# Performance work log

Measured on AMD Instinct MI355X. Metric: run time of the kernel, lower is better.

The kernel has to match this reference:

```python
import jax, jax.numpy as jnp
import numpy as np


def setup_inputs() -> dict:
    key = jax.random.key(0)
    ks = jax.random.split(key, 7)
    T, K, D_x, D_y = 8192, 64, 128, 64
    X = jax.random.normal(ks[0], (T, D_x), dtype=jnp.float32)
    Y = jax.random.normal(ks[1], (T, D_y), dtype=jnp.float32)
    # learned parameters (small random values for non-degenerate math)
    init_logits = jax.random.normal(ks[2], (K,), dtype=jnp.float32) * 0.1
    W = jax.random.normal(ks[3], (K, K, D_x), dtype=jnp.float32) * 0.05
    b = jax.random.normal(ks[4], (K, K), dtype=jnp.float32) * 0.1
    mu = jax.random.normal(ks[5], (K, D_y), dtype=jnp.float32) * 0.1
    log_var_unconstrained = jax.random.normal(ks[6], (K, D_y), dtype=jnp.float32) * 0.1
    return {"X": X, "Y": Y, "init_logits": init_logits, "W": W, "b": b,
            "mu": mu, "log_var_unconstrained": log_var_unconstrained}


def reference(X, Y, init_logits, W, b, mu, log_var_unconstrained):
    # log pi0
    log_pi0 = jax.nn.log_softmax(init_logits)
    # emissions for all t: diagonal Gaussian log-pdf, log_em [T, K]
    log_var = jnp.clip(log_var_unconstrained, -6.0, 6.0)  # [K, D_y]
    D = Y.shape[-1]
    LOG2PI = jnp.log(jnp.asarray(2.0 * np.pi, dtype=Y.dtype))
    diff = Y[:, None, :] - mu[None, :, :]                 # [T, K, D_y]
    quad = jnp.sum(diff * diff * jnp.exp(-log_var)[None], axis=-1)  # [T, K]
    logdet = jnp.sum(log_var, axis=-1)                    # [K]
    log_em = -0.5 * (D * LOG2PI + logdet[None, :] + quad)  # [T, K]
    # time-varying transition logits: b_ij + x_t . W_ij, row-softmax over j
    logits = b[None, :, :] + jnp.einsum('ijd,td->tij', W, X)  # [T, K, K]
    log_A = jax.nn.log_softmax(logits, axis=2)                 # [T, K, K]
    # forward recursion: alpha_t(j) = log_em_t(j) + logsumexp_i(alpha_{t-1}(i) + log_A_t(i,j))
    alpha0 = log_pi0 + log_em[0]

    def step(alpha, inputs):
        log_A_t, log_em_t = inputs
        alpha_new = log_em_t + jax.nn.logsumexp(alpha[:, None] + log_A_t, axis=0)
        return alpha_new, None

    alpha_T, _ = jax.lax.scan(step, alpha0, (log_A[1:], log_em[1:]))
    loglik = jax.nn.logsumexp(alpha_T)
    return loglik
```

## Files before the change

### kernel.cpp

```cpp
#include <hip/hip_runtime.h>
#include <hip/hip_bf16.h>


typedef unsigned int u32;
typedef unsigned short u16;

#define T_LEN 8192

typedef __attribute__((ext_vector_type(8))) short bf16x8;
typedef __attribute__((ext_vector_type(4))) float f32x4;

__device__ __forceinline__ float bflo(u32 u){ return __uint_as_float(u << 16); }
__device__ __forceinline__ float bfhi(u32 u){ return __uint_as_float(u & 0xffff0000u); }
__device__ __forceinline__ u32 f2bf(float x){
  u32 b = __float_as_uint(x);
  return (b + 0x7fffu + ((b >> 16) & 1u)) >> 16;
}
__device__ __forceinline__ u32 pack2bf(float a, float b){
  return f2bf(a) | (f2bf(b) << 16);
}

__device__ __forceinline__ void gld_lds16(const void* g, void* l){
#if defined(__has_builtin) && __has_builtin(__builtin_amdgcn_global_load_lds)
  __builtin_amdgcn_global_load_lds(
      (const __attribute__((address_space(1))) unsigned int*)g,
      (__attribute__((address_space(3))) unsigned int*)l, 16, 0, 0);
#else
  *(uint4*)((char*)l + (threadIdx.x & 63) * 16) = *(const uint4*)g;
#endif
}

__global__ __launch_bounds__(64) void k_prep(
    const float* __restrict__ mu, const float* __restrict__ lvu,
    float* __restrict__ muT, float* __restrict__ ivT, float* __restrict__ logdet)
{
  const int k = threadIdx.x;
  float ld = 0.f;
  for (int d = 0; d < 64; ++d){
    float lv = fminf(fmaxf(lvu[k*64 + d], -6.f), 6.f);
    ld += lv;
    muT[d*64 + k] = mu[k*64 + d];
    ivT[d*64 + k] = __expf(-lv);
  }
  logdet[k] = ld;
}

__global__ __launch_bounds__(256) void k_emis(
    const float* __restrict__ Y, const float* __restrict__ muT,
    const float* __restrict__ ivT, const float* __restrict__ logdet,
    const float* __restrict__ X, const float* __restrict__ W,
    float* __restrict__ emp, float* __restrict__ cvec,
    u16* __restrict__ Xsw, u16* __restrict__ Wsw)
{
  const int tid = threadIdx.x;
  const int w = tid >> 6, k = tid & 63;
  const int t = blockIdx.x * 4 + w;
  float y = Y[(size_t)t*64 + k];
  float quad = 0.f;
  #pragma unroll 8
  for (int d = 0; d < 64; ++d){
    float yd = __shfl(y, d, 64);
    float df = yd - muT[d*64 + k];
    quad = fmaf(df*df, ivT[d*64 + k], quad);
  }
  float le = -0.5f*(117.6241322f + logdet[k] + quad);
  float m = le;
  #pragma unroll
  for (int off = 1; off < 64; off <<= 1) m = fmaxf(m, __shfl_xor(m, off, 64));
  emp[(size_t)t*64 + k] = __expf(le - m);
  if (k == 0) cvec[t] = m;

  if (tid < 128){
    int rl = tid >> 5, c32 = tid & 31;
    int tr = blockIdx.x*4 + rl;
    float4 v = *(const float4*)(X + (size_t)tr*128 + c32*4);
    int c16 = c32 >> 1, h = c32 & 1;
    int byte = tr*256 + ((c16 ^ (tr & 7))*16 + h*8);
    *(uint2*)((char*)Xsw + byte) = make_uint2(pack2bf(v.x,v.y), pack2bf(v.z,v.w));
  }
  if (blockIdx.x < 512){
    int f4 = blockIdx.x*256 + tid;
    int r = f4 >> 5, c32 = f4 & 31;
    float4 v = *(const float4*)(W + (size_t)f4*4);
    int c16 = c32 >> 1, h = c32 & 1;
    int byte = r*256 + ((c16 ^ (r & 7))*16 + h*8);
    *(uint2*)((char*)Wsw + byte) = make_uint2(pack2bf(v.x,v.y), pack2bf(v.z,v.w));
  }
}

__global__ __launch_bounds__(256) void k_trans(
    const u16* __restrict__ Xsw, const u16* __restrict__ Wsw,
    const float* __restrict__ bmat, const float* __restrict__ emp,
    u16* __restrict__ Ap)
{
  __shared__ __align__(16) u16 Wt[128*128];
  __shared__ __align__(16) u16 Xt[64*128];
  __shared__ float Sred[8][64];
  const int tid = threadIdx.x;
  const int lane = tid & 63, w = tid >> 6;
  const int lr = lane & 15, lg = lane >> 4;
  const int t0 = blockIdx.x * 64;
  const int i0 = blockIdx.y * 2;

  {
    const char* xsrc = (const char*)(Xsw + (size_t)t0*128);
    const char* wsrc = (const char*)(Wsw + (size_t)i0*64*128);
    #pragma unroll
    for (int c = 0; c < 4; ++c){
      int kb = w*4 + c;
      gld_lds16(xsrc + kb*1024 + lane*16, (char*)Xt + kb*1024);
    }
    #pragma unroll
    for (int c = 0; c < 8; ++c){
      int kb = w*8 + c;
      gld_lds16(wsrc + kb*1024 + lane*16, (char*)Wt + kb*1024);
    }
  }
  __syncthreads();

  f32x4 acc[2][4] = {};
  #pragma unroll
  for (int kg = 0; kg < 4; ++kg){
    const int kc = kg*4 + lg;
    bf16x8 a[2], b[4];
    #pragma unroll
    for (int jt = 0; jt < 2; ++jt){
      int row = (w + jt*4)*16 + lr;
      a[jt] = *(const bf16x8*)((const char*)Wt + row*256 + ((kc ^ (row & 7))*16));
    }
    #pragma unroll
    for (int tt = 0; tt < 4; ++tt){
      int row = tt*16 + lr;
      b[tt] = *(const bf16x8*)((const char*)Xt + row*256 + ((kc ^ (row & 7))*16));
    }
    #pragma unroll
    for (int jt = 0; jt < 2; ++jt)
      #pragma unroll
      for (int tt = 0; tt < 4; ++tt)
        acc[jt][tt] = __builtin_amdgcn_mfma_f32_16x16x32_bf16(a[jt], b[tt], acc[jt][tt], 0, 0, 0);
  }

  float bvv[2][4];
  #pragma unroll
  for (int jt = 0; jt < 2; ++jt){
    int q = w + jt*4;
    int ig = i0 + (q >> 2);
    #pragma unroll
    for (int reg = 0; reg < 4; ++reg)
      bvv[jt][reg] = bmat[ig*64 + (q & 3)*16 + lg*4 + reg];
  }

  __syncthreads();
  u16* Ct = Xt;

  #pragma unroll
  for (int jt = 0; jt < 2; ++jt){
    const int q = w + jt*4;
    #pragma unroll
    for (int tt = 0; tt < 4; ++tt){
      const int t = tt*16 + lr;
      float e0 = __expf(acc[jt][tt][0] + bvv[jt][0]);
      float e1 = __expf(acc[jt][tt][1] + bvv[jt][1]);
      float e2 = __expf(acc[jt][tt][2] + bvv[jt][2]);
      float e3 = __expf(acc[jt][tt][3] + bvv[jt][3]);
      float s = e0 + e1 + e2 + e3;
      s += __shfl_xor(s, 16, 64);
      s += __shfl_xor(s, 32, 64);
      if (lg == 0) Sred[q][t] = s;
      const int byte = t*256 + ((q*32 + lg*8) ^ ((t & 7) << 4));
      *(u32*)((char*)Ct + byte)     = pack2bf(e0, e1);
      *(u32*)((char*)Ct + byte + 4) = pack2bf(e2, e3);
    }
  }
  __syncthreads();

  {
    const int trow = tid >> 2, seg = tid & 3;
    float invs[2];
    #pragma unroll
    for (int ii = 0; ii < 2; ++ii){
      float s = Sred[ii*4+0][trow] + Sred[ii*4+1][trow]
              + Sred[ii*4+2][trow] + Sred[ii*4+3][trow];
      invs[ii] = 1.0f / s;
    }
    const int sw = (trow & 7) << 4;
    u16* orow = Ap + (size_t)(t0 + trow)*4096 + i0*64;
    const float* er = emp + (size_t)(t0 + trow)*64;
    #pragma unroll
    for (int u = 0; u < 4; ++u){
      const int bcol = seg*64 + u*16;
      uint4 v = *(const uint4*)((const char*)Ct + trow*256 + (bcol ^ sw));
      const int j0 = bcol >> 1;
      const float inv = invs[j0 >> 6];
      const int je = j0 & 63;
      float4 ea = *(const float4*)(er + je);
      float4 eb = *(const float4*)(er + je + 4);
      u32 r0 = pack2bf(bflo(v.x)*inv*ea.x, bfhi(v.x)*inv*ea.y);
      u32 r1 = pack2bf(bflo(v.y)*inv*ea.z, bfhi(v.y)*inv*ea.w);
      u32 r2 = pack2bf(bflo(v.z)*inv*eb.x, bfhi(v.z)*inv*eb.y);
      u32 r3 = pack2bf(bflo(v.w)*inv*eb.z, bfhi(v.w)*inv*eb.w);
      *(uint4*)(orow + j0) = make_uint4(r0, r1, r2, r3);
    }
  }
}

__global__ __launch_bounds__(256) void k_scan(
    u16* mats, int mstride, int per_wg, int skip0,
    const float* __restrict__ in_sc, float* __restrict__ out_sc)
{
  __shared__ u32 Apk[2][32*68];
  const int tid = threadIdx.x;
  const int lane = tid & 63, w = tid >> 6;
  const int r16 = lane & 15, oct = lane >> 4;
  int c0 = blockIdx.x * per_wg, cnt = per_wg;
  const size_t out_slot = (size_t)c0 * mstride;
  if (blockIdx.x == 0){ c0 += skip0; cnt -= skip0; }

  bf16x8 Bf[2];
  {
    const u16* m0 = mats + ((size_t)c0*mstride << 12) + (w*16 + r16)*64 + oct*8;
    Bf[0] = *(const bf16x8*)(m0);
    Bf[1] = *(const bf16x8*)(m0 + 32);
  }
  float S = in_sc ? in_sc[c0*4 + w] : 0.0f;

  const int lp = tid >> 3, c8 = tid & 7;
  auto STAGE = [&](int buf, const u16* src){
    const uint4 A = *(const uint4*)(src + lp*128 + c8*8);
    const uint4 B = *(const uint4*)(src + lp*128 + 64 + c8*8);
    uint4 o0, o1;
    o0.x = (A.x & 0xffffu) | (B.x << 16);
    o0.y = (A.x >> 16)     | (B.x & 0xffff0000u);
    o0.z = (A.y & 0xffffu) | (B.y << 16);
    o0.w = (A.y >> 16)     | (B.y & 0xffff0000u);
    o1.x = (A.z & 0xffffu) | (B.z << 16);
    o1.y = (A.z >> 16)     | (B.z & 0xffff0000u);
    o1.z = (A.w & 0xffffu) | (B.w << 16);
    o1.w = (A.w >> 16)     | (B.w & 0xffff0000u);
    u32* dst = &Apk[buf][lp*68 + c8*8];
    *(uint4*)(dst)     = o0;
    *(uint4*)(dst + 4) = o1;
  };

  if (cnt > 1) STAGE(0, mats + ((size_t)(c0+1)*mstride << 12));
  __syncthreads();
  int cur = 0;
  for (int kk = 1; kk < cnt; ++kk){
    if (kk + 1 < cnt) STAGE(cur ^ 1, mats + ((size_t)(c0 + kk + 1)*mstride << 12));

    if (in_sc){
      const float* sp = in_sc + (size_t)(c0 + kk)*4;
      float s0=sp[0], s1=sp[1], s2=sp[2], s3=sp[3];
      float sm = fmaxf(fmaxf(s0,s1), fmaxf(s2,s3));
      S += sm;
      #pragma unroll
      for (int kt = 0; kt < 2; ++kt){
        float slo = (kt == 0) ? s0 : s2;
        float shi = (kt == 0) ? s1 : s3;
        float se = __expf(((oct >> 1) ? shi : slo) - sm);
        uint4 bv4 = __builtin_bit_cast(uint4, Bf[kt]);
        bv4.x = pack2bf(bflo(bv4.x)*se, bfhi(bv4.x)*se);
        bv4.y = pack2bf(bflo(bv4.y)*se, bfhi(bv4.y)*se);
        bv4.z = pack2bf(bflo(bv4.z)*se, bfhi(bv4.z)*se);
        bv4.w = pack2bf(bflo(bv4.w)*se, bfhi(bv4.w)*se);
        Bf[kt] = __builtin_bit_cast(bf16x8, bv4);
      }
    }

    f32x4 acc[4] = {};
    const u32* Ab = &Apk[cur][0];
    #pragma unroll
    for (int kt = 0; kt < 2; ++kt){
      const u32* gb = Ab + (kt*16 + oct*4)*68 + r16;
      #pragma unroll
      for (int jt = 0; jt < 4; ++jt){
        const u32* g = gb + jt*16;
        uint4 av = make_uint4(g[0], g[68], g[136], g[204]);
        acc[jt] = __builtin_amdgcn_mfma_f32_16x16x32_bf16(
            __builtin_bit_cast(bf16x8, av), Bf[kt], acc[jt], 0, 0, 0);
      }
    }

    float mx = acc[0][0];
    #pragma unroll
    for (int jt = 0; jt < 4; ++jt)
      #pragma unroll
      for (int q = 0; q < 4; ++q) mx = fmaxf(mx, acc[jt][q]);
    #pragma unroll
    for (int off = 1; off < 64; off <<= 1) mx = fmaxf(mx, __shfl_xor(mx, off, 64));
    float inv = 1.0f / mx;
    S += __logf(mx);

    u32 p0[4], p1[4];
    #pragma unroll
    for (int jt = 0; jt < 4; ++jt){
      p0[jt] = pack2bf(acc[jt][0]*inv, acc[jt][1]*inv);
      p1[jt] = pack2bf(acc[jt][2]*inv, acc[jt][3]*inv);
    }
    const int s0l = r16 + 32*(oct & 1), s1l = s0l + 16;
    const bool hi = (oct >> 1) != 0;
    #pragma unroll
    for (int kt = 0; kt < 2; ++kt){
      u32 a0 = __shfl(p0[2*kt],   s0l, 64), a1 = __shfl(p1[2*kt],   s0l, 64);
      u32 a2 = __shfl(p0[2*kt],   s1l, 64), a3 = __shfl(p1[2*kt],   s1l, 64);
      u32 b0 = __shfl(p0[2*kt+1], s0l, 64), b1 = __shfl(p1[2*kt+1], s0l, 64);
      u32 b2 = __shfl(p0[2*kt+1], s1l, 64), b3 = __shfl(p1[2*kt+1], s1l, 64);
      uint4 nb;
      nb.x = hi ? b0 : a0;
      nb.y = hi ? b1 : a1;
      nb.z = hi ? b2 : a2;
      nb.w = hi ? b3 : a3;
      Bf[kt] = __builtin_bit_cast(bf16x8, nb);
    }
    cur ^= 1;
    __syncthreads();
  }
  {
    u16* outp = mats + (out_slot << 12) + (w*16 + r16)*64 + oct*8;
    *(bf16x8*)(outp)      = Bf[0];
    *(bf16x8*)(outp + 32) = Bf[1];
    if (lane == 0) out_sc[blockIdx.x*4 + w] = S;
  }
}

__global__ __launch_bounds__(256) void k_final(
    const float* __restrict__ init_logits, const float* __restrict__ emp,
    const float* __restrict__ cvec, const u16* __restrict__ Mfin, int mstride,
    const float* __restrict__ scfin, int nmat, float* __restrict__ out)
{
  __shared__ float wsum[4];
  const int tid = threadIdx.x;
  float part = 0.f;
  for (int t = tid; t < T_LEN; t += 256) part += cvec[t];
  #pragma unroll
  for (int off = 1; off < 64; off <<= 1) part += __shfl_xor(part, off, 64);
  if ((tid & 63) == 0) wsum[tid >> 6] = part;
  __syncthreads();
  if (tid >= 64) return;
  const float csum = wsum[0] + wsum[1] + wsum[2] + wsum[3];
  const int k = tid;
  float ilv = init_logits[k];
  float m = ilv;
  #pragma unroll
  for (int off = 1; off < 64; off <<= 1) m = fmaxf(m, __shfl_xor(m, off, 64));
  float e = __expf(ilv - m);
  float s = e;
  #pragma unroll
  for (int off = 1; off < 64; off <<= 1) s += __shfl_xor(s, off, 64);
  float alpha = (e / s) * emp[k];
  float S = 0.f;
  for (int d = 0; d < nmat; ++d){
    const float* sp = scfin + d*4;
    float sm = fmaxf(fmaxf(sp[0], sp[1]), fmaxf(sp[2], sp[3]));
    alpha *= __expf(sp[k >> 4] - sm);
    S += sm;
    const u16* Mp = Mfin + ((size_t)d*mstride << 12);
    float an = 0.f;
    for (int i2 = 0; i2 < 64; ++i2){
      float av = __shfl(alpha, i2, 64);
      an = fmaf(av, __uint_as_float(((u32)Mp[i2*64 + k]) << 16), an);
    }
    float mx = an;
    #pragma unroll
    for (int off = 1; off < 64; off <<= 1) mx = fmaxf(mx, __shfl_xor(mx, off, 64));
    alpha = an / mx;
    S += __logf(mx);
  }
  float tot = alpha;
  #pragma unroll
  for (int off = 1; off < 64; off <<= 1) tot += __shfl_xor(tot, off, 64);
  if (k == 0) out[0] = __logf(tot) + S + csum;
}

extern "C" void kernel_launch(void* const* d_in, const int* in_sizes, int n_in,
                              void* d_out, int out_size, void* d_ws, size_t ws_size,
                              hipStream_t stream)
{
  const float* X  = (const float*)d_in[0];
  const float* Y  = (const float*)d_in[1];
  const float* il = (const float*)d_in[2];
  const float* W  = (const float*)d_in[3];
  const float* bm = (const float*)d_in[4];
  const float* mu = (const float*)d_in[5];
  const float* lv = (const float*)d_in[6];
  float* out = (float*)d_out;
  char* ws = (char*)d_ws;
  (void)in_sizes; (void)n_in; (void)out_size; (void)ws_size;

  float* emp    = (float*)(ws + 0x0000000);
  float* cvec   = (float*)(ws + 0x0200000);
  float* muT    = (float*)(ws + 0x0210000);
  float* ivT    = (float*)(ws + 0x0214000);
  float* logdet = (float*)(ws + 0x0218000);
  float* sc1    = (float*)(ws + 0x0220000);
  float* sc2    = (float*)(ws + 0x0224000);
  float* sc3    = (float*)(ws + 0x0225000);
  float* sc4    = (float*)(ws + 0x0226000);
  u16*   Xsw    = (u16*)  (ws + 0x0240000);
  u16*   Wsw    = (u16*)  (ws + 0x0440000);
  u16*   Ap     = (u16*)  (ws + 0x0600000);

  k_prep <<<1, 64, 0, stream>>>(mu, lv, muT, ivT, logdet);
  k_emis <<<2048, 256, 0, stream>>>(Y, muT, ivT, logdet, X, W, emp, cvec, Xsw, Wsw);
  k_trans<<<dim3(128, 32), 256, 0, stream>>>(Xsw, Wsw, bm, emp, Ap);
  k_scan <<<1024, 256, 0, stream>>>(Ap,   1,  8, 1, (const float*)nullptr, sc1);
  k_scan <<<128,  256, 0, stream>>>(Ap,   8,  8, 0, sc1, sc2);
  k_scan <<<16,   256, 0, stream>>>(Ap,  64,  8, 0, sc2, sc3);
  k_scan <<<1,    256, 0, stream>>>(Ap, 512, 16, 0, sc3, sc4);
  k_final<<<1, 256, 0, stream>>>(il, emp, cvec, Ap, 1, sc4, 1, out);
}
```

Measured before the change: 205.2 us.

## Fuse scan levels into one cooperative kernel, fold prep into emission kernel

The four scan-level launches and the final kernel are merged into one cooperative kernel that uses grid-wide syncs between tree levels, with the old multi-launch path kept as a fallback if the cooperative launch fails. The separate prep kernel is removed: each emission block now rebuilds transposed mu and inverse variances in shared memory. The transition kernel's epilogue is remapped so each wave writes contiguous 16-byte chunks of rows. The aim is to cut launch gaps and the single-block prep kernel, at the cost of redundant per-block prep work and grid-sync overhead with mostly idle blocks at the upper levels.

```diff
diff --git a/kernel.cpp b/kernel.cpp
--- a/kernel.cpp
+++ b/kernel.cpp
@@ -1,6 +1,9 @@
 #include <hip/hip_runtime.h>
 #include <hip/hip_bf16.h>
-
+#include <hip/hip_cooperative_groups.h>
+
+
+namespace cg = cooperative_groups;
 
 typedef unsigned int u32;
 typedef unsigned short u16;
@@ -30,40 +33,52 @@
 #endif
 }
 
-__global__ __launch_bounds__(64) void k_prep(
-    const float* __restrict__ mu, const float* __restrict__ lvu,
-    float* __restrict__ muT, float* __restrict__ ivT, float* __restrict__ logdet)
-{
-  const int k = threadIdx.x;
-  float ld = 0.f;
-  for (int d = 0; d < 64; ++d){
-    float lv = fminf(fmaxf(lvu[k*64 + d], -6.f), 6.f);
-    ld += lv;
-    muT[d*64 + k] = mu[k*64 + d];
-    ivT[d*64 + k] = __expf(-lv);
-  }
-  logdet[k] = ld;
-}
-
 __global__ __launch_bounds__(256) void k_emis(
-    const float* __restrict__ Y, const float* __restrict__ muT,
-    const float* __restrict__ ivT, const float* __restrict__ logdet,
+    const float* __restrict__ Y, const float* __restrict__ mu,
+    const float* __restrict__ lvu,
     const float* __restrict__ X, const float* __restrict__ W,
     float* __restrict__ emp, float* __restrict__ cvec,
     u16* __restrict__ Xsw, u16* __restrict__ Wsw)
 {
+  __shared__ float muT_s[64][65];
+  __shared__ float ivT_s[64][65];
   const int tid = threadIdx.x;
   const int w = tid >> 6, k = tid & 63;
+
+  #pragma unroll
+  for (int u = 0; u < 4; ++u){
+    int f4 = u*256 + tid;
+    int r = f4 >> 4, c4 = (f4 & 15) * 4;
+    float4 m4 = *(const float4*)(mu + (size_t)f4*4);
+    float4 l4 = *(const float4*)(lvu + (size_t)f4*4);
+    muT_s[c4+0][r] = m4.x; muT_s[c4+1][r] = m4.y;
+    muT_s[c4+2][r] = m4.z; muT_s[c4+3][r] = m4.w;
+    ivT_s[c4+0][r] = fminf(fmaxf(l4.x, -6.f), 6.f);
+    ivT_s[c4+1][r] = fminf(fmaxf(l4.y, -6.f), 6.f);
+    ivT_s[c4+2][r] = fminf(fmaxf(l4.z, -6.f), 6.f);
+    ivT_s[c4+3][r] = fminf(fmaxf(l4.w, -6.f), 6.f);
+  }
+  __syncthreads();
+  float ld = 0.f;
+  #pragma unroll 8
+  for (int d = 0; d < 64; ++d) ld += ivT_s[d][k];
+  __syncthreads();
+  if (w == 0){
+    #pragma unroll 8
+    for (int d = 0; d < 64; ++d) ivT_s[d][k] = __expf(-ivT_s[d][k]);
+  }
+  __syncthreads();
+
   const int t = blockIdx.x * 4 + w;
   float y = Y[(size_t)t*64 + k];
   float quad = 0.f;
   #pragma unroll 8
   for (int d = 0; d < 64; ++d){
     float yd = __shfl(y, d, 64);
-    float df = yd - muT[d*64 + k];
-    quad = fmaf(df*df, ivT[d*64 + k], quad);
-  }
-  float le = -0.5f*(117.6241322f + logdet[k] + quad);
+    float df = yd - muT_s[d][k];
+    quad = fmaf(df*df, ivT_s[d][k], quad);
+  }
+  float le = -0.5f*(117.6241322f + ld + quad);
   float m = le;
   #pragma unroll
   for (int off = 1; off < 64; off <<= 1) m = fmaxf(m, __shfl_xor(m, off, 64));
@@ -175,46 +190,36 @@
   __syncthreads();
 
   {
-    const int trow = tid >> 2, seg = tid & 3;
-    float invs[2];
-    #pragma unroll
-    for (int ii = 0; ii < 2; ++ii){
-      float s = Sred[ii*4+0][trow] + Sred[ii*4+1][trow]
-              + Sred[ii*4+2][trow] + Sred[ii*4+3][trow];
-      invs[ii] = 1.0f / s;
-    }
-    const int sw = (trow & 7) << 4;
-    u16* orow = Ap + (size_t)(t0 + trow)*4096 + i0*64;
-    const float* er = emp + (size_t)(t0 + trow)*64;
+    const int rl = lane >> 4;
+    const int ch = lane & 15;
+    const int h = ch >> 3;
     #pragma unroll
     for (int u = 0; u < 4; ++u){
-      const int bcol = seg*64 + u*16;
-      uint4 v = *(const uint4*)((const char*)Ct + trow*256 + (bcol ^ sw));
-      const int j0 = bcol >> 1;
-      const float inv = invs[j0 >> 6];
-      const int je = j0 & 63;
-      float4 ea = *(const float4*)(er + je);
-      float4 eb = *(const float4*)(er + je + 4);
+      const int row = w*16 + u*4 + rl;
+      float s = Sred[h*4+0][row] + Sred[h*4+1][row]
+              + Sred[h*4+2][row] + Sred[h*4+3][row];
+      const float inv = 1.0f / s;
+      uint4 v = *(const uint4*)((const char*)Ct + row*256 + ((ch*16) ^ ((row & 7) << 4)));
+      const float* er = emp + (size_t)(t0 + row)*64 + (ch & 7)*8;
+      float4 ea = *(const float4*)(er);
+      float4 eb = *(const float4*)(er + 4);
       u32 r0 = pack2bf(bflo(v.x)*inv*ea.x, bfhi(v.x)*inv*ea.y);
       u32 r1 = pack2bf(bflo(v.y)*inv*ea.z, bfhi(v.y)*inv*ea.w);
       u32 r2 = pack2bf(bflo(v.z)*inv*eb.x, bfhi(v.z)*inv*eb.y);
       u32 r3 = pack2bf(bflo(v.w)*inv*eb.z, bfhi(v.w)*inv*eb.w);
-      *(uint4*)(orow + j0) = make_uint4(r0, r1, r2, r3);
-    }
-  }
-}
-
-__global__ __launch_bounds__(256) void k_scan(
-    u16* mats, int mstride, int per_wg, int skip0,
-    const float* __restrict__ in_sc, float* __restrict__ out_sc)
-{
-  __shared__ u32 Apk[2][32*68];
-  const int tid = threadIdx.x;
+      *(uint4*)(Ap + (size_t)(t0 + row)*4096 + (size_t)i0*64 + ch*8) = make_uint4(r0, r1, r2, r3);
+    }
+  }
+}
+
+__device__ void fold_chunk(
+    u16* mats, int c0_in, int mstride, int cnt_in, int skip,
+    const float* in_sc, float* out_sc, int tid, u32 (&Apk)[2][32*68])
+{
   const int lane = tid & 63, w = tid >> 6;
   const int r16 = lane & 15, oct = lane >> 4;
-  int c0 = blockIdx.x * per_wg, cnt = per_wg;
-  const size_t out_slot = (size_t)c0 * mstride;
-  if (blockIdx.x == 0){ c0 += skip0; cnt -= skip0; }
+  int c0 = c0_in + skip, cnt = cnt_in - skip;
+  const size_t out_slot = (size_t)c0_in * mstride;
 
   bf16x8 Bf[2];
   {
@@ -319,17 +324,15 @@
     u16* outp = mats + (out_slot << 12) + (w*16 + r16)*64 + oct*8;
     *(bf16x8*)(outp)      = Bf[0];
     *(bf16x8*)(outp + 32) = Bf[1];
-    if (lane == 0) out_sc[blockIdx.x*4 + w] = S;
-  }
-}
-
-__global__ __launch_bounds__(256) void k_final(
-    const float* __restrict__ init_logits, const float* __restrict__ emp,
-    const float* __restrict__ cvec, const u16* __restrict__ Mfin, int mstride,
-    const float* __restrict__ scfin, int nmat, float* __restrict__ out)
+    if (lane == 0) out_sc[w] = S;
+  }
+}
+
+__device__ void final_ll(
+    const float* init_logits, const float* emp, const float* cvec,
+    const u16* Mfin, const float* scfin, float* out, int tid)
 {
   __shared__ float wsum[4];
-  const int tid = threadIdx.x;
   float part = 0.f;
   for (int t = tid; t < T_LEN; t += 256) part += cvec[t];
   #pragma unroll
@@ -348,28 +351,56 @@
   #pragma unroll
   for (int off = 1; off < 64; off <<= 1) s += __shfl_xor(s, off, 64);
   float alpha = (e / s) * emp[k];
-  float S = 0.f;
-  for (int d = 0; d < nmat; ++d){
-    const float* sp = scfin + d*4;
-    float sm = fmaxf(fmaxf(sp[0], sp[1]), fmaxf(sp[2], sp[3]));
-    alpha *= __expf(sp[k >> 4] - sm);
-    S += sm;
-    const u16* Mp = Mfin + ((size_t)d*mstride << 12);
-    float an = 0.f;
-    for (int i2 = 0; i2 < 64; ++i2){
-      float av = __shfl(alpha, i2, 64);
-      an = fmaf(av, __uint_as_float(((u32)Mp[i2*64 + k]) << 16), an);
-    }
-    float mx = an;
-    #pragma unroll
-    for (int off = 1; off < 64; off <<= 1) mx = fmaxf(mx, __shfl_xor(mx, off, 64));
-    alpha = an / mx;
-    S += __logf(mx);
-  }
-  float tot = alpha;
+  const float* sp = scfin;
+  float sm = fmaxf(fmaxf(sp[0], sp[1]), fmaxf(sp[2], sp[3]));
+  alpha *= __expf(sp[k >> 4] - sm);
+  float S = sm;
+  float an = 0.f;
+  for (int i2 = 0; i2 < 64; ++i2){
+    float av = __shfl(alpha, i2, 64);
+    an = fmaf(av, __uint_as_float(((u32)Mfin[i2*64 + k]) << 16), an);
+  }
+  float tot = an;
   #pragma unroll
   for (int off = 1; off < 64; off <<= 1) tot += __shfl_xor(tot, off, 64);
   if (k == 0) out[0] = __logf(tot) + S + csum;
+}
+
+__global__ __launch_bounds__(256, 4) void k_scanall(
+    u16* mats, const float* init_logits, const float* emp, const float* cvec,
+    float* sc1, float* sc2, float* sc3, float* sc4, float* out)
+{
+  __shared__ u32 Apk[2][32*68];
+  cg::grid_group grid = cg::this_grid();
+  const int b = blockIdx.x;
+  const int tid = threadIdx.x;
+  fold_chunk(mats, b*8, 1, 8, (b == 0) ? 1 : 0, nullptr, sc1 + b*4, tid, Apk);
+  grid.sync();
+  if (b < 128) fold_chunk(mats, b*8, 8, 8, 0, sc1, sc2 + b*4, tid, Apk);
+  grid.sync();
+  if (b < 16) fold_chunk(mats, b*8, 64, 8, 0, sc2, sc3 + b*4, tid, Apk);
+  grid.sync();
+  if (b == 0) fold_chunk(mats, 0, 512, 16, 0, sc3, sc4, tid, Apk);
+  grid.sync();
+  if (b == 0) final_ll(init_logits, emp, cvec, mats, sc4, out, tid);
+}
+
+__global__ __launch_bounds__(256) void k_scan_lvl(
+    u16* mats, int mstride, int per_wg, int skip0,
+    const float* __restrict__ in_sc, float* __restrict__ out_sc)
+{
+  __shared__ u32 Apk[2][32*68];
+  const int b = blockIdx.x;
+  fold_chunk(mats, b*per_wg, mstride, per_wg, (b == 0) ? skip0 : 0,
+             in_sc, out_sc + b*4, threadIdx.x, Apk);
+}
+
+__global__ __launch_bounds__(256) void k_final_k(
+    const float* __restrict__ init_logits, const float* __restrict__ emp,
+    const float* __restrict__ cvec, const u16* __restrict__ Mfin,
+    const float* __restrict__ scfin, float* __restrict__ out)
+{
+  final_ll(init_logits, emp, cvec, Mfin, scfin, out, threadIdx.x);
 }
 
 extern "C" void kernel_launch(void* const* d_in, const int* in_sizes, int n_in,
@@ -387,25 +418,28 @@
   char* ws = (char*)d_ws;
   (void)in_sizes; (void)n_in; (void)out_size; (void)ws_size;
 
-  float* emp    = (float*)(ws + 0x0000000);
-  float* cvec   = (float*)(ws + 0x0200000);
-  float* muT    = (float*)(ws + 0x0210000);
-  float* ivT    = (float*)(ws + 0x0214000);
-  float* logdet = (float*)(ws + 0x0218000);
-  float* sc1    = (float*)(ws + 0x0220000);
-  float* sc2    = (float*)(ws + 0x0224000);
-  float* sc3    = (float*)(ws + 0x0225000);
-  float* sc4    = (float*)(ws + 0x0226000);
-  u16*   Xsw    = (u16*)  (ws + 0x0240000);
-  u16*   Wsw    = (u16*)  (ws + 0x0440000);
-  u16*   Ap     = (u16*)  (ws + 0x0600000);
-
-  k_prep <<<1, 64, 0, stream>>>(mu, lv, muT, ivT, logdet);
-  k_emis <<<2048, 256, 0, stream>>>(Y, muT, ivT, logdet, X, W, emp, cvec, Xsw, Wsw);
+  float* emp  = (float*)(ws + 0x0000000);
+  float* cvec = (float*)(ws + 0x0200000);
+  float* sc1  = (float*)(ws + 0x0220000);
+  float* sc2  = (float*)(ws + 0x0224000);
+  float* sc3  = (float*)(ws + 0x0225000);
+  float* sc4  = (float*)(ws + 0x0226000);
+  u16*   Xsw  = (u16*)  (ws + 0x0240000);
+  u16*   Wsw  = (u16*)  (ws + 0x0440000);
+  u16*   Ap   = (u16*)  (ws + 0x0600000);
+
+  k_emis <<<2048, 256, 0, stream>>>(Y, mu, lv, X, W, emp, cvec, Xsw, Wsw);
   k_trans<<<dim3(128, 32), 256, 0, stream>>>(Xsw, Wsw, bm, emp, Ap);
-  k_scan <<<1024, 256, 0, stream>>>(Ap,   1,  8, 1, (const float*)nullptr, sc1);
-  k_scan <<<128,  256, 0, stream>>>(Ap,   8,  8, 0, sc1, sc2);
-  k_scan <<<16,   256, 0, stream>>>(Ap,  64,  8, 0, sc2, sc3);
-  k_scan <<<1,    256, 0, stream>>>(Ap, 512, 16, 0, sc3, sc4);
-  k_final<<<1, 256, 0, stream>>>(il, emp, cvec, Ap, 1, sc4, 1, out);
-}
+
+  void* args[] = {(void*)&Ap, (void*)&il, (void*)&emp, (void*)&cvec,
+                  (void*)&sc1, (void*)&sc2, (void*)&sc3, (void*)&sc4, (void*)&out};
+  hipError_t rc = hipLaunchCooperativeKernel((void*)k_scanall, dim3(1024), dim3(256),
+                                             args, 0, stream);
+  if (rc != hipSuccess){
+    k_scan_lvl<<<1024, 256, 0, stream>>>(Ap,   1,  8, 1, (const float*)nullptr, sc1);
+    k_scan_lvl<<<128,  256, 0, stream>>>(Ap,   8,  8, 0, sc1, sc2);
+    k_scan_lvl<<<16,   256, 0, stream>>>(Ap,  64,  8, 0, sc2, sc3);
+    k_scan_lvl<<<1,    256, 0, stream>>>(Ap, 512, 16, 0, sc3, sc4);
+    k_final_k <<<1,    256, 0, stream>>>(il, emp, cvec, Ap, sc4, out);
+  }
+}
```

After: 632.3 us. +208.2%, slower.
